# Kernel optimization log

Hardware: AMD Instinct MI355X
Metric: run time of the kernel (lower is better)

## Reference

```python
import jax, jax.numpy as jnp
import numpy as np

B, D, UNITS, C = 16384, 1024, 1500, 2000  # batch, embed_dim, leaves, total classes
N_NORM = 2.0
EPS = 1e-6


def setup_inputs() -> dict:
    key = jax.random.key(0)
    k_in, k_w, k_r = jax.random.split(key, 3)
    inputs = jax.random.normal(k_in, (B, D), dtype=jnp.float32)
    # glorot init for linear (embedding_dim, units)
    scale = jnp.sqrt(6.0 / (D + UNITS)).astype(jnp.float32)
    linear = jax.random.uniform(k_w, (D, UNITS), dtype=jnp.float32, minval=-scale, maxval=scale)
    bias = jnp.zeros((UNITS,), dtype=jnp.float32)
    # R_t: (n_classes, units) 0/1 ancestor mask. Leaf classes (first UNITS rows)
    # map to themselves (identity); internal classes get random leaf descendants.
    leaf_rows = jnp.eye(UNITS, dtype=jnp.float32)
    anc_rows = (jax.random.uniform(k_r, (C - UNITS, UNITS)) < 0.05).astype(jnp.float32)
    R_t = jnp.concatenate([leaf_rows, anc_rows], axis=0)
    return {"inputs": inputs, "linear": linear, "bias": bias, "R_t": R_t}


def reference(inputs, linear, bias, R_t):
    # sigmoid linear layer: (B, UNITS)
    out = jax.nn.sigmoid(inputs @ linear + bias)
    # n>1 branch: n_norm(out[:, None, :] * R_t).
    # Because R_t is a 0/1 mask, (out_j * R_t[c, j])**n == R_t[c, j] * out_j**n,
    # so the broadcast-multiply + pow + sum fuses exactly into a masked matmul.
    s = (out ** N_NORM) @ R_t.T               # (B, C) = sum over leaves
    s = jnp.clip(s, EPS, 1.0 - EPS)
    return s ** (1.0 / N_NORM)
```

## Files before the change

kernel.cpp:

```cpp
#include <hip/hip_runtime.h>
#include <stdint.h>

#define BROWS 16384
#define DDIM 1024
#define UNITSN 1500
#define UNITSP 1536
#define CCLS 2000
#define NINT 500
#define NINTP 512
#define EPSV 1e-6f
#define LEAF_LO 1e-3f
#define LEAF_HI 0.9999995f

typedef __bf16 bf16x8 __attribute__((ext_vector_type(8)));
typedef float f32x4 __attribute__((ext_vector_type(4)));
typedef unsigned short u16x4v __attribute__((ext_vector_type(4)));

__device__ __forceinline__ unsigned short f2bf(float f) {
  union { float f; uint32_t u; } x; x.f = f;
  uint32_t r = x.u + 0x7fffu + ((x.u >> 16) & 1u);
  return (unsigned short)(r >> 16);
}

__device__ __forceinline__ float fast_rcp(float x) {
  float r; asm("v_rcp_f32 %0, %1" : "=v"(r) : "v"(x)); return r;
}
__device__ __forceinline__ float fast_sqrt(float x) {
  float r; asm("v_sqrt_f32 %0, %1" : "=v"(r) : "v"(x)); return r;
}

__device__ __forceinline__ void gload_lds16(const void* g, void* l) {
  __builtin_amdgcn_global_load_lds(
      reinterpret_cast<const __attribute__((address_space(1))) void*>(
          reinterpret_cast<uintptr_t>(g)),
      reinterpret_cast<__attribute__((address_space(3))) void*>(
          (uint32_t)reinterpret_cast<uintptr_t>(l)),
      16, 0, 0);
}

#define VMW(n) asm volatile("s_waitcnt vmcnt(" #n ")" ::: "memory")
#define LGKM0() asm volatile("s_waitcnt lgkmcnt(0)" ::: "memory")
#define SBAR() __builtin_amdgcn_s_barrier()
#define SCHED0() __builtin_amdgcn_sched_barrier(0)
#define MFMA __builtin_amdgcn_mfma_f32_16x16x32_bf16

__global__ __launch_bounds__(256) void k_prep(
    const float* __restrict__ inputs, const float* __restrict__ lin,
    const float* __restrict__ R, unsigned short* __restrict__ Ab,
    unsigned short* __restrict__ wt, unsigned short* __restrict__ Rb) {
  const int b = blockIdx.x, t = threadIdx.x;

  if (b < 1536) {
    __shared__ float tle[32][33];
    const int nb = (b % 48) * 32;
    const int kb = (b / 48) * 32;
    const int tx = t & 31, ty = t >> 5;
#pragma unroll
    for (int s = 0; s < 32; s += 8) {
      int k = kb + ty + s, n = nb + tx;
      tle[ty + s][tx] = (n < UNITSN) ? lin[k * UNITSN + n] : 0.f;
    }
    __syncthreads();
#pragma unroll
    for (int s = 0; s < 32; s += 8) {
      int n = nb + ty + s, k = kb + tx;
      wt[n * DDIM + k] = f2bf(tle[tx][ty + s]);
    }
  }

  const int gtid = b * 256 + t;
  const float4* in4 = (const float4*)inputs;
  for (int i = gtid; i < (BROWS * DDIM) / 4; i += 2048 * 256) {
    float4 v = in4[i];
    u16x4v o;
    o.x = f2bf(v.x); o.y = f2bf(v.y); o.z = f2bf(v.z); o.w = f2bf(v.w);
    *reinterpret_cast<u16x4v*>(Ab + i * 4) = o;
  }

  for (int i = gtid; i < NINTP * UNITSP; i += 2048 * 256) {
    int r = i / UNITSP;
    int u = i - r * UNITSP;
    float v = (r < NINT && u < UNITSN) ? R[(size_t)(UNITSN + r) * UNITSN + u] : 0.f;
    Rb[i] = f2bf(v);
  }
}

__global__ __launch_bounds__(512, 4) void k_gemm1(
    const unsigned short* __restrict__ A,
    const unsigned short* __restrict__ Bt,
    const float* __restrict__ bias,
    unsigned short* __restrict__ o2,
    float* __restrict__ outf) {
  constexpr int K = DDIM;
  constexpr int NKT = K / 32;
  constexpr int NBX = 12;
  __shared__ char smem[65536];

  const int nwg = (int)gridDim.x;
  const int qx = nwg >> 3;
  const int bid = (int)blockIdx.x;
  const int wg = (bid & 7) * qx + (bid >> 3);
  const int bx = wg % NBX, by = wg / NBX;
  const int brow = by << 7, bcol = bx << 7;

  const int tid = (int)threadIdx.x;
  const int lane = tid & 63;
  const int w = tid >> 6;
  const int wr = w >> 2, wc = w & 3;

  const int srow = tid >> 2;
  const int skc = tid & 3;
  const unsigned short* gA = A + (size_t)(brow + srow) * K + ((skc ^ (srow & 3)) << 3);
  const unsigned short* gB = Bt + (size_t)(bcol + srow) * K + ((skc ^ (srow & 3)) << 3);
  const int sW = w << 10;

  const int chnk = ((lane >> 4) ^ (lane & 3)) << 4;
  const int aOff = (((wr << 6) + (lane & 15)) << 6) + chnk;
  const int bOff = 8192 + ((((wc << 5) + (lane & 15))) << 6) + chnk;

#define STG(bS, gt) do { \
    gload_lds16(gA + (size_t)(gt) * 32, smem + (bS) * 16384 + sW); \
    gload_lds16(gB + (size_t)(gt) * 32, smem + (bS) * 16384 + 8192 + sW); \
  } while (0)
#define LDA1(b, i) (*reinterpret_cast<const bf16x8*>(smem + (b) * 16384 + aOff + (i) * 1024))
#define LDB1(b, j) (*reinterpret_cast<const bf16x8*>(smem + (b) * 16384 + bOff + (j) * 1024))

  f32x4 acc[4][2] = {};

  STG(0, 0); STG(1, 1); STG(2, 2);
  VMW(4);
  SBAR(); SCHED0();

#define TILE(bR, bS, gt, DOSTG, VMWSTMT) { \
    bf16x8 a0 = LDA1(bR, 0), a1 = LDA1(bR, 1), a2 = LDA1(bR, 2), a3 = LDA1(bR, 3); \
    bf16x8 b0 = LDB1(bR, 0), b1 = LDB1(bR, 1); \
    if (DOSTG) { STG(bS, gt); } \
    LGKM0(); VMWSTMT; \
    SBAR(); SCHED0(); \
    __builtin_amdgcn_s_setprio(1); \
    acc[0][0] = MFMA(a0, b0, acc[0][0], 0, 0, 0); \
    acc[1][0] = MFMA(a1, b0, acc[1][0], 0, 0, 0); \
    acc[2][0] = MFMA(a2, b0, acc[2][0], 0, 0, 0); \
    acc[3][0] = MFMA(a3, b0, acc[3][0], 0, 0, 0); \
    acc[0][1] = MFMA(a0, b1, acc[0][1], 0, 0, 0); \
    acc[1][1] = MFMA(a1, b1, acc[1][1], 0, 0, 0); \
    acc[2][1] = MFMA(a2, b1, acc[2][1], 0, 0, 0); \
    acc[3][1] = MFMA(a3, b1, acc[3][1], 0, 0, 0); \
    __builtin_amdgcn_s_setprio(0); \
  }

  for (int it = 0; it < 7; ++it) {
    const int t = it << 2;
    TILE(0, 3, t + 3, 1, VMW(4));
    TILE(1, 0, t + 4, 1, VMW(4));
    TILE(2, 1, t + 5, 1, VMW(4));
    TILE(3, 2, t + 6, 1, VMW(4));
  }
  TILE(0, 3, 31, 1, VMW(4));
  TILE(1, 0, 0, 0, VMW(2));
  TILE(2, 0, 0, 0, VMW(0));
  TILE(3, 0, 0, 0, (void)0);
#undef TILE
#undef STG
#undef LDA1
#undef LDB1

#pragma unroll
  for (int i = 0; i < 4; ++i) {
    const int row0 = brow + (wr << 6) + i * 16 + ((lane >> 4) << 2);
#pragma unroll
    for (int j = 0; j < 2; ++j) {
      const int col = bcol + (wc << 5) + j * 16 + (lane & 15);
      const bool live = (col < UNITSN);
      float bz = live ? bias[col] : 0.f;
#pragma unroll
      for (int r = 0; r < 4; ++r) {
        float z = acc[i][j][r] + bz;
        float sg = fast_rcp(1.f + __expf(-z));
        float s2 = sg * sg;
        o2[(size_t)(row0 + r) * UNITSP + col] = f2bf(live ? s2 : 0.f);
        if (live) {
          outf[(size_t)(row0 + r) * CCLS + col] = fminf(fmaxf(sg, LEAF_LO), LEAF_HI);
        }
      }
    }
  }
}

template <int NBX, int K>
__global__ __launch_bounds__(512, 4) void k_g128i(
    const unsigned short* __restrict__ A,
    const unsigned short* __restrict__ Bt,
    float* __restrict__ outf) {
  constexpr int NKT = K / 64;
  constexpr int BUFS = 32768;
  __shared__ char smem[2 * BUFS];

  const int nwg = (int)gridDim.x;
  const int qx = nwg >> 3;
  const int bid = (int)blockIdx.x;
  const int wg = (bid & 7) * qx + (bid >> 3);
  const int bx = wg % NBX, by = wg / NBX;
  const int brow = by << 7, bcol = bx << 7;

  const int tid = (int)threadIdx.x;
  const int lane = tid & 63;
  const int w = tid >> 6;
  const int wr = w >> 2, wc = w & 3;

  const unsigned short* gA =
      A + (size_t)(brow + (w << 3) + (lane >> 3)) * K + (((lane & 7) ^ (lane >> 3)) << 3);
  const unsigned short* gB =
      Bt + (size_t)(bcol + (w << 3) + (lane >> 3)) * K + (((lane & 7) ^ (lane >> 3)) << 3);
  const int sW = w << 10;

  const int s0 = (((lane >> 4) ^ (lane & 7)) << 4);
  const int aRB = (((wr << 6) + (lane & 15)) << 7);
  const int bRB = 16384 + (((wc << 5) + (lane & 15)) << 7);

#define STA2(b, u, gt) gload_lds16(gA + (size_t)((u) * 64) * K + (size_t)(gt) * 64, \
                                   smem + ((b) * BUFS + (u) * 8192) + sW)
#define STB2(b, u, gt) gload_lds16(gB + (size_t)((u) * 64) * K + (size_t)(gt) * 64, \
                                   smem + ((b) * BUFS + 16384 + (u) * 8192) + sW)
#define LDA2(b, i, ks) (*reinterpret_cast<const bf16x8*>( \
    smem + (b) * BUFS + aRB + (i) * 2048 + (s0 ^ ((ks) * 64))))
#define LDB2(b, j, ks) (*reinterpret_cast<const bf16x8*>( \
    smem + (b) * BUFS + bRB + (j) * 2048 + (s0 ^ ((ks) * 64))))

  f32x4 acc[4][2] = {};
  bf16x8 Bf0[2], Bf1[2];

  STB2(0, 0, 0); STB2(0, 1, 0);
  STA2(0, 0, 0); STA2(0, 1, 0);
  STB2(1, 0, 1); STB2(1, 1, 1);
  VMW(2);
  SBAR(); SCHED0();

  for (int it = 0; it < NKT / 2; ++it) {
    const int tb = 2 * it + 1, t2 = 2 * it + 2, t3 = 2 * it + 3;
    {
      bf16x8 a00 = LDA2(0, 0, 0), a01 = LDA2(0, 0, 1);
      bf16x8 a10 = LDA2(0, 1, 0), a11 = LDA2(0, 1, 1);
#pragma unroll
      for (int j = 0; j < 2; ++j) { Bf0[j] = LDB2(0, j, 0); Bf1[j] = LDB2(0, j, 1); }
      STA2(1, 0, tb); STA2(1, 1, tb);
      SBAR(); LGKM0(); SCHED0();
      __builtin_amdgcn_s_setprio(1);
#pragma unroll
      for (int j = 0; j < 2; ++j) { acc[0][j] = MFMA(a00, Bf0[j], acc[0][j], 0, 0, 0);
                                    acc[1][j] = MFMA(a10, Bf0[j], acc[1][j], 0, 0, 0); }
#pragma unroll
      for (int j = 0; j < 2; ++j) { acc[0][j] = MFMA(a01, Bf1[j], acc[0][j], 0, 0, 0);
                                    acc[1][j] = MFMA(a11, Bf1[j], acc[1][j], 0, 0, 0); }
      __builtin_amdgcn_s_setprio(0);
      SBAR(); SCHED0();
    }
    {
      bf16x8 a00 = LDA2(0, 2, 0), a01 = LDA2(0, 2, 1);
      bf16x8 a10 = LDA2(0, 3, 0), a11 = LDA2(0, 3, 1);
      if (t2 < NKT) { STB2(0, 0, t2); STB2(0, 1, t2); }
      SBAR(); LGKM0(); SCHED0();
      __builtin_amdgcn_s_setprio(1);
#pragma unroll
      for (int j = 0; j < 2; ++j) { acc[2][j] = MFMA(a00, Bf0[j], acc[2][j], 0, 0, 0);
                                    acc[3][j] = MFMA(a10, Bf0[j], acc[3][j], 0, 0, 0); }
#pragma unroll
      for (int j = 0; j < 2; ++j) { acc[2][j] = MFMA(a01, Bf1[j], acc[2][j], 0, 0, 0);
                                    acc[3][j] = MFMA(a11, Bf1[j], acc[3][j], 0, 0, 0); }
      __builtin_amdgcn_s_setprio(0);
      if (t2 < NKT) { VMW(2); } else { VMW(0); }
      SBAR(); SCHED0();
    }
    {
      bf16x8 a00 = LDA2(1, 0, 0), a01 = LDA2(1, 0, 1);
      bf16x8 a10 = LDA2(1, 1, 0), a11 = LDA2(1, 1, 1);
#pragma unroll
      for (int j = 0; j < 2; ++j) { Bf0[j] = LDB2(1, j, 0); Bf1[j] = LDB2(1, j, 1); }
      if (t2 < NKT) { STA2(0, 0, t2); STA2(0, 1, t2); }
      SBAR(); LGKM0(); SCHED0();
      __builtin_amdgcn_s_setprio(1);
#pragma unroll
      for (int j = 0; j < 2; ++j) { acc[0][j] = MFMA(a00, Bf0[j], acc[0][j], 0, 0, 0);
                                    acc[1][j] = MFMA(a10, Bf0[j], acc[1][j], 0, 0, 0); }
#pragma unroll
      for (int j = 0; j < 2; ++j) { acc[0][j] = MFMA(a01, Bf1[j], acc[0][j], 0, 0, 0);
                                    acc[1][j] = MFMA(a11, Bf1[j], acc[1][j], 0, 0, 0); }
      __builtin_amdgcn_s_setprio(0);
      SBAR(); SCHED0();
    }
    {
      bf16x8 a00 = LDA2(1, 2, 0), a01 = LDA2(1, 2, 1);
      bf16x8 a10 = LDA2(1, 3, 0), a11 = LDA2(1, 3, 1);
      if (t3 < NKT) { STB2(1, 0, t3); STB2(1, 1, t3); }
      SBAR(); LGKM0(); SCHED0();
      __builtin_amdgcn_s_setprio(1);
#pragma unroll
      for (int j = 0; j < 2; ++j) { acc[2][j] = MFMA(a00, Bf0[j], acc[2][j], 0, 0, 0);
                                    acc[3][j] = MFMA(a10, Bf0[j], acc[3][j], 0, 0, 0); }
#pragma unroll
      for (int j = 0; j < 2; ++j) { acc[2][j] = MFMA(a01, Bf1[j], acc[2][j], 0, 0, 0);
                                    acc[3][j] = MFMA(a11, Bf1[j], acc[3][j], 0, 0, 0); }
      __builtin_amdgcn_s_setprio(0);
      if (t3 < NKT) { VMW(2); }
      SBAR(); SCHED0();
    }
  }

#pragma unroll
  for (int i = 0; i < 4; ++i) {
    const int row0 = brow + (wr << 6) + i * 16 + ((lane >> 4) << 2);
#pragma unroll
    for (int j = 0; j < 2; ++j) {
      const int col = bcol + (wc << 5) + j * 16 + (lane & 15);
      if (col < NINT) {
#pragma unroll
        for (int r = 0; r < 4; ++r) {
          float s = acc[i][j][r];
          s = fminf(fmaxf(s, EPSV), 1.f - EPSV);
          outf[(size_t)(row0 + r) * CCLS + UNITSN + col] = fast_sqrt(s);
        }
      }
    }
  }
#undef STA2
#undef STB2
#undef LDA2
#undef LDB2
}


extern "C" void kernel_launch(void* const* d_in, const int* in_sizes, int n_in,
                              void* d_out, int out_size, void* d_ws, size_t ws_size,
                              hipStream_t stream) {
  const float* inputs = (const float*)d_in[0];
  const float* linear = (const float*)d_in[1];
  const float* bias   = (const float*)d_in[2];
  const float* R_t    = (const float*)d_in[3];
  float* out = (float*)d_out;

  char* ws = (char*)d_ws;
  unsigned short* Ab  = (unsigned short*)(ws);
  unsigned short* Wt  = (unsigned short*)(ws + 33554432);
  unsigned short* RbI = (unsigned short*)(ws + 36700160);
  unsigned short* O2  = (unsigned short*)(ws + 38273024);

  k_prep<<<2048, 256, 0, stream>>>(inputs, linear, R_t, Ab, Wt, RbI);

  k_gemm1<<<1536, 512, 0, stream>>>(Ab, Wt, bias, O2, out);
  k_g128i<4, UNITSP><<<512, 512, 0, stream>>>(O2, RbI, out);
}
```

Measured before the change: 126.9 us.

## Load GEMM1 B operand directly into registers and deepen K-step to 64

The first GEMM kernel stops staging the weight (B) tile through LDS and instead has each wave load its B fragments straight from global memory into double-buffered registers. The whole 16KB LDS stage now holds a 128x64 A tile, so each barrier covers a K=64 step (16 steps instead of 32) with 16 MFMAs, and the swizzle widens to 8 chunks. The aim is fewer barriers and less LDS traffic per MFMA. The cost is more register pressure and uncoalesced, less-shared global reads for B, since each wave of the block fetches its own B slice.

```diff
diff --git a/kernel.cpp b/kernel.cpp
--- a/kernel.cpp
+++ b/kernel.cpp
@@ -85,14 +85,13 @@
   }
 }
 
-__global__ __launch_bounds__(512, 4) void k_gemm1(
+__global__ __launch_bounds__(512, 4) void k_gemm1b(
     const unsigned short* __restrict__ A,
     const unsigned short* __restrict__ Bt,
     const float* __restrict__ bias,
     unsigned short* __restrict__ o2,
     float* __restrict__ outf) {
   constexpr int K = DDIM;
-  constexpr int NKT = K / 32;
   constexpr int NBX = 12;
   __shared__ char smem[65536];
 
@@ -108,62 +107,85 @@
   const int w = tid >> 6;
   const int wr = w >> 2, wc = w & 3;
 
-  const int srow = tid >> 2;
-  const int skc = tid & 3;
-  const unsigned short* gA = A + (size_t)(brow + srow) * K + ((skc ^ (srow & 3)) << 3);
-  const unsigned short* gB = Bt + (size_t)(bcol + srow) * K + ((skc ^ (srow & 3)) << 3);
+  const int srow = tid >> 3;
+  const int skc = tid & 7;
+  const unsigned short* gA0 =
+      A + (size_t)(brow + srow) * K + ((skc ^ (srow & 7)) << 3);
+  const unsigned short* gA1 = gA0 + (size_t)64 * K;
   const int sW = w << 10;
 
-  const int chnk = ((lane >> 4) ^ (lane & 3)) << 4;
-  const int aOff = (((wr << 6) + (lane & 15)) << 6) + chnk;
-  const int bOff = 8192 + ((((wc << 5) + (lane & 15))) << 6) + chnk;
-
-#define STG(bS, gt) do { \
-    gload_lds16(gA + (size_t)(gt) * 32, smem + (bS) * 16384 + sW); \
-    gload_lds16(gB + (size_t)(gt) * 32, smem + (bS) * 16384 + 8192 + sW); \
+  const int aBase = (((wr << 6) + (lane & 15)) << 7) + (((lane >> 4) ^ (lane & 7)) << 4);
+
+  const unsigned short* pB0 =
+      Bt + (size_t)(bcol + (wc << 5) + (lane & 15)) * K + ((lane >> 4) << 3);
+  const unsigned short* pB1 = pB0 + (size_t)16 * K;
+
+#define STG(bs, t) do { \
+    gload_lds16(gA0 + (size_t)(t) * 64, smem + (bs) * 16384 + sW); \
+    gload_lds16(gA1 + (size_t)(t) * 64, smem + (bs) * 16384 + 8192 + sW); \
   } while (0)
-#define LDA1(b, i) (*reinterpret_cast<const bf16x8*>(smem + (b) * 16384 + aOff + (i) * 1024))
-#define LDB1(b, j) (*reinterpret_cast<const bf16x8*>(smem + (b) * 16384 + bOff + (j) * 1024))
+#define LDA1(p, i, ks) (*reinterpret_cast<const bf16x8*>( \
+    smem + (p) * 16384 + (aBase ^ ((ks) * 64)) + (i) * 2048))
+#define LB(pp, ks, t) (*reinterpret_cast<const bf16x8*>((pp) + (t) * 64 + (ks) * 32))
 
   f32x4 acc[4][2] = {};
-
+  bf16x8 BX0, BX1, BX2, BX3, BY0, BY1, BY2, BY3;
+
+  BX0 = LB(pB0, 0, 0); BX1 = LB(pB0, 1, 0); BX2 = LB(pB1, 0, 0); BX3 = LB(pB1, 1, 0);
   STG(0, 0); STG(1, 1); STG(2, 2);
   VMW(4);
   SBAR(); SCHED0();
 
-#define TILE(bR, bS, gt, DOSTG, VMWSTMT) { \
-    bf16x8 a0 = LDA1(bR, 0), a1 = LDA1(bR, 1), a2 = LDA1(bR, 2), a3 = LDA1(bR, 3); \
-    bf16x8 b0 = LDB1(bR, 0), b1 = LDB1(bR, 1); \
-    if (DOSTG) { STG(bS, gt); } \
-    LGKM0(); VMWSTMT; \
+#define TILEX(p, t3, DO_STG, t1, DO_B, VMSTMT, BC0, BC1, BC2, BC3, BN0, BN1, BN2, BN3) { \
+    bf16x8 a00 = LDA1(p, 0, 0), a01 = LDA1(p, 0, 1); \
+    bf16x8 a10 = LDA1(p, 1, 0), a11 = LDA1(p, 1, 1); \
+    bf16x8 a20 = LDA1(p, 2, 0), a21 = LDA1(p, 2, 1); \
+    bf16x8 a30 = LDA1(p, 3, 0), a31 = LDA1(p, 3, 1); \
+    if (DO_B) { BN0 = LB(pB0, 0, t1); BN1 = LB(pB0, 1, t1); \
+                BN2 = LB(pB1, 0, t1); BN3 = LB(pB1, 1, t1); } \
+    if (DO_STG) { STG((t3) & 3, t3); } \
+    LGKM0(); VMSTMT; \
     SBAR(); SCHED0(); \
     __builtin_amdgcn_s_setprio(1); \
-    acc[0][0] = MFMA(a0, b0, acc[0][0], 0, 0, 0); \
-    acc[1][0] = MFMA(a1, b0, acc[1][0], 0, 0, 0); \
-    acc[2][0] = MFMA(a2, b0, acc[2][0], 0, 0, 0); \
-    acc[3][0] = MFMA(a3, b0, acc[3][0], 0, 0, 0); \
-    acc[0][1] = MFMA(a0, b1, acc[0][1], 0, 0, 0); \
-    acc[1][1] = MFMA(a1, b1, acc[1][1], 0, 0, 0); \
-    acc[2][1] = MFMA(a2, b1, acc[2][1], 0, 0, 0); \
-    acc[3][1] = MFMA(a3, b1, acc[3][1], 0, 0, 0); \
+    acc[0][0] = MFMA(a00, BC0, acc[0][0], 0, 0, 0); \
+    acc[1][0] = MFMA(a10, BC0, acc[1][0], 0, 0, 0); \
+    acc[2][0] = MFMA(a20, BC0, acc[2][0], 0, 0, 0); \
+    acc[3][0] = MFMA(a30, BC0, acc[3][0], 0, 0, 0); \
+    acc[0][1] = MFMA(a00, BC2, acc[0][1], 0, 0, 0); \
+    acc[1][1] = MFMA(a10, BC2, acc[1][1], 0, 0, 0); \
+    acc[2][1] = MFMA(a20, BC2, acc[2][1], 0, 0, 0); \
+    acc[3][1] = MFMA(a30, BC2, acc[3][1], 0, 0, 0); \
+    acc[0][0] = MFMA(a01, BC1, acc[0][0], 0, 0, 0); \
+    acc[1][0] = MFMA(a11, BC1, acc[1][0], 0, 0, 0); \
+    acc[2][0] = MFMA(a21, BC1, acc[2][0], 0, 0, 0); \
+    acc[3][0] = MFMA(a31, BC1, acc[3][0], 0, 0, 0); \
+    acc[0][1] = MFMA(a01, BC3, acc[0][1], 0, 0, 0); \
+    acc[1][1] = MFMA(a11, BC3, acc[1][1], 0, 0, 0); \
+    acc[2][1] = MFMA(a21, BC3, acc[2][1], 0, 0, 0); \
+    acc[3][1] = MFMA(a31, BC3, acc[3][1], 0, 0, 0); \
     __builtin_amdgcn_s_setprio(0); \
   }
 
-  for (int it = 0; it < 7; ++it) {
-    const int t = it << 2;
-    TILE(0, 3, t + 3, 1, VMW(4));
-    TILE(1, 0, t + 4, 1, VMW(4));
-    TILE(2, 1, t + 5, 1, VMW(4));
-    TILE(3, 2, t + 6, 1, VMW(4));
-  }
-  TILE(0, 3, 31, 1, VMW(4));
-  TILE(1, 0, 0, 0, VMW(2));
-  TILE(2, 0, 0, 0, VMW(0));
-  TILE(3, 0, 0, 0, (void)0);
-#undef TILE
+  TILEX(0,  3, 1,  1, 1, VMW(8),  BX0, BX1, BX2, BX3, BY0, BY1, BY2, BY3);
+  TILEX(1,  4, 1,  2, 1, VMW(12), BY0, BY1, BY2, BY3, BX0, BX1, BX2, BX3);
+  TILEX(2,  5, 1,  3, 1, VMW(12), BX0, BX1, BX2, BX3, BY0, BY1, BY2, BY3);
+  TILEX(3,  6, 1,  4, 1, VMW(12), BY0, BY1, BY2, BY3, BX0, BX1, BX2, BX3);
+  TILEX(0,  7, 1,  5, 1, VMW(12), BX0, BX1, BX2, BX3, BY0, BY1, BY2, BY3);
+  TILEX(1,  8, 1,  6, 1, VMW(12), BY0, BY1, BY2, BY3, BX0, BX1, BX2, BX3);
+  TILEX(2,  9, 1,  7, 1, VMW(12), BX0, BX1, BX2, BX3, BY0, BY1, BY2, BY3);
+  TILEX(3, 10, 1,  8, 1, VMW(12), BY0, BY1, BY2, BY3, BX0, BX1, BX2, BX3);
+  TILEX(0, 11, 1,  9, 1, VMW(12), BX0, BX1, BX2, BX3, BY0, BY1, BY2, BY3);
+  TILEX(1, 12, 1, 10, 1, VMW(12), BY0, BY1, BY2, BY3, BX0, BX1, BX2, BX3);
+  TILEX(2, 13, 1, 11, 1, VMW(12), BX0, BX1, BX2, BX3, BY0, BY1, BY2, BY3);
+  TILEX(3, 14, 1, 12, 1, VMW(12), BY0, BY1, BY2, BY3, BX0, BX1, BX2, BX3);
+  TILEX(0, 15, 1, 13, 1, VMW(12), BX0, BX1, BX2, BX3, BY0, BY1, BY2, BY3);
+  TILEX(1,  0, 0, 14, 1, VMW(10), BY0, BY1, BY2, BY3, BX0, BX1, BX2, BX3);
+  TILEX(2,  0, 0, 15, 1, VMW(8),  BX0, BX1, BX2, BX3, BY0, BY1, BY2, BY3);
+  TILEX(3,  0, 0,  0, 0, (void)0, BY0, BY1, BY2, BY3, BX0, BX1, BX2, BX3);
+#undef TILEX
 #undef STG
 #undef LDA1
-#undef LDB1
+#undef LB
 
 #pragma unroll
   for (int i = 0; i < 4; ++i) {
@@ -346,6 +368,6 @@
 
   k_prep<<<2048, 256, 0, stream>>>(inputs, linear, R_t, Ab, Wt, RbI);
 
-  k_gemm1<<<1536, 512, 0, stream>>>(Ab, Wt, bias, O2, out);
+  k_gemm1b<<<1536, 512, 0, stream>>>(Ab, Wt, bias, O2, out);
   k_g128i<4, UNITSP><<<512, 512, 0, stream>>>(O2, RbI, out);
 }
```

After: 161.1 us. 1.27x slower.
